# Kernel optimization log

Measured on AMD Instinct MI355X. Metric: run time of the kernel, lower is better.

## Reference

```python
import jax, jax.numpy as jnp
import numpy as np

EMBED_DIM = 1024
NUM_HEADS = 16
HEAD_DIM = EMBED_DIM // NUM_HEADS


def setup_inputs() -> dict:
    key = jax.random.key(0)
    ks = jax.random.split(key, 7)
    B, N, C = 2, 2048, EMBED_DIM
    s = 1.0 / np.sqrt(C)
    return {
        "x": jax.random.normal(ks[0], (B, N, C), dtype=jnp.float32),
        "phase_signal": jax.random.uniform(ks[1], (B,), dtype=jnp.float32),
        "qkv_w": jax.random.normal(ks[2], (3 * C, C), dtype=jnp.float32) * s,
        "qkv_b": jnp.zeros((3 * C,), dtype=jnp.float32),
        "proj_w": jax.random.normal(ks[3], (C, C), dtype=jnp.float32) * s,
        "proj_b": jnp.zeros((C,), dtype=jnp.float32),
        "phase_weight": jnp.ones((NUM_HEADS,), dtype=jnp.float32),
    }


def reference(x, phase_signal, qkv_w, qkv_b, proj_w, proj_b, phase_weight):
    B, N, C = x.shape
    H, D = NUM_HEADS, HEAD_DIM
    # qkv projection: [B,N,3C] -> [3,B,H,N,D]
    qkv = (x @ qkv_w.T + qkv_b).reshape(B, N, 3, H, D)
    qkv = jnp.transpose(qkv, (2, 0, 3, 1, 4))
    q, k, v = qkv[0], qkv[1], qkv[2]
    attn = jnp.einsum("bhnd,bhmd->bhnm", q, k) * (D ** -0.5)
    # per-(batch, head) phase modulation applied before softmax
    phase_mod = phase_weight[None, :, None, None] * phase_signal[:, None, None, None]
    attn = attn * (1.0 + 0.2 * phase_mod)
    attn = jax.nn.softmax(attn, axis=-1)  # dropout is identity in eval mode
    out = jnp.einsum("bhnm,bhmd->bhnd", attn, v)
    out = jnp.transpose(out, (0, 2, 1, 3)).reshape(B, N, C)
    return out @ proj_w.T + proj_b
```

## Files before the change

### kernel.cpp

```cpp
#include <hip/hip_runtime.h>
#include <stdint.h>

#define NUM_H 16
#define HD    64
#define CDIM  1024
#define NSEQ  2048
#define NBATCH 2
#define LOG2E 1.4426950408889634f

typedef __attribute__((ext_vector_type(8))) short short8;
typedef __attribute__((ext_vector_type(4))) float f32x4;
typedef __attribute__((ext_vector_type(16))) float f32x16;
typedef __attribute__((ext_vector_type(4))) unsigned short ushort4v;
typedef __attribute__((ext_vector_type(4))) float float4v;
typedef __attribute__((ext_vector_type(2))) unsigned int u32x2;

__device__ __forceinline__ unsigned short f2bf(float f) {
    unsigned int u = __builtin_bit_cast(unsigned int, f);
    unsigned int r = u + 0x7fffu + ((u >> 16) & 1u);
    return (unsigned short)(r >> 16);
}

__device__ __forceinline__ float bf2f(unsigned short u) {
    return __builtin_bit_cast(float, (unsigned int)u << 16);
}

__device__ __forceinline__ unsigned int cvtpk(float a, float b) {
    unsigned int r;
    asm("v_cvt_pk_bf16_f32 %0, %1, %2" : "=v"(r) : "v"(a), "v"(b));
    return r;
}

__device__ __forceinline__ void plswap(unsigned int &a, unsigned int &b) {
    asm("v_permlane32_swap_b32 %0, %1" : "+v"(a), "+v"(b));
}

__device__ __forceinline__ void gload_lds16(const void* g, const void* l) {
    __builtin_amdgcn_global_load_lds(
        (const __attribute__((address_space(1))) unsigned int*)(unsigned long long)(uintptr_t)g,
        (__attribute__((address_space(3))) unsigned int*)(unsigned int)(uintptr_t)l,
        16, 0, 0);
}

__global__ void cvt_all_kernel(const float* __restrict__ x,
                               const float* __restrict__ w1,
                               const float* __restrict__ wp,
                               unsigned short* __restrict__ xo,
                               unsigned short* __restrict__ w1o,
                               unsigned short* __restrict__ wpo) {
    int i = blockIdx.x * blockDim.x + threadIdx.x;
    const float* in; unsigned short* out;
    if (i < 1048576)      { in = x;  out = xo; }
    else if (i < 1835008) { in = w1; out = w1o; i -= 1048576; }
    else                  { in = wp; out = wpo; i -= 1835008; }
    float4v v = *(const float4v*)(in + (size_t)i * 4);
    ushort4v o;
    o[0] = f2bf(v[0]); o[1] = f2bf(v[1]); o[2] = f2bf(v[2]); o[3] = f2bf(v[3]);
    *(ushort4v*)(out + (size_t)i * 4) = o;
}

__global__ __launch_bounds__(512, 2) void gemm_qkv(
    const unsigned short* __restrict__ A,
    const unsigned short* __restrict__ Bw,
    const float* __restrict__ bias,
    const float* __restrict__ ps,
    const float* __restrict__ pw,
    unsigned short* __restrict__ qb,
    unsigned short* __restrict__ kfrag,
    unsigned short* __restrict__ vfrag)
{
    __shared__ unsigned short lds[2][2][2][128][64];

    const int tid = threadIdx.x;
    const int wid = tid >> 6;
    const int lane = tid & 63;
    const int l15 = lane & 15, l4 = lane >> 4;
    const int wave_m = wid >> 2, wave_n = wid & 3;

    const int bm = blockIdx.x;
    const int bn = blockIdx.y;

    f32x4 acc[8][4];
    const f32x4 zero4 = {0.f, 0.f, 0.f, 0.f};
#pragma unroll
    for (int m = 0; m < 8; ++m)
#pragma unroll
        for (int n = 0; n < 4; ++n) acc[m][n] = zero4;

    const int jr = lane >> 3;
    const int jc = ((lane & 7) ^ jr) << 4;
    const char* aB = (const char*)A  + (size_t)(bm * 256) * 2048;
    const char* bB = (const char*)Bw + (size_t)(bn * 256) * 2048;

    auto stageH = [&](int t, int which) {
        const int buf = t & 1;
        const int op = which >> 1, hf = which & 1;
        const char* src = (op == 0) ? aB : bB;
        const int rowb = hf * 128 + wid * 16;
        const size_t k0b = (size_t)t * 128;
        char* dst = (char*)&lds[buf][op][hf][wid * 16][0];
#pragma unroll
        for (int i = 0; i < 2; ++i)
            gload_lds16(src + (size_t)(rowb + i * 8 + jr) * 2048 + k0b + jc,
                        dst + i * 1024);
    };

    const int swz = (l15 & 7) << 4;
    auto rdA = [&](int buf, int mq, int mp, int kk) -> short8 {
        return *(const short8*)((const char*)&lds[buf][0][wave_m][mq * 64 + mp * 16 + l15][0]
                                + ((kk * 64 + l4 * 16) ^ swz));
    };
    auto rdB = [&](int buf, int nq, int np, int kk) -> short8 {
        const int br = wave_n * 64 + nq * 32 + np * 16 + l15;
        return *(const short8*)((const char*)&lds[buf][1][br >> 7][br & 127][0]
                                + ((kk * 64 + l4 * 16) ^ swz));
    };

    stageH(0, 0); stageH(0, 1); stageH(0, 2); stageH(0, 3);
    stageH(1, 2); stageH(1, 3); stageH(1, 0); stageH(1, 1);
    asm volatile("s_waitcnt vmcnt(8)" ::: "memory");
    __builtin_amdgcn_s_barrier();

    for (int t = 0; t < 16; ++t) {
        const int buf = t & 1;
        short8 af[4][2], bf[2][2][2];

#pragma unroll
        for (int mp = 0; mp < 4; ++mp) {
            af[mp][0] = rdA(buf, 0, mp, 0); af[mp][1] = rdA(buf, 0, mp, 1);
        }
#pragma unroll
        for (int np = 0; np < 2; ++np) {
            bf[0][np][0] = rdB(buf, 0, np, 0); bf[0][np][1] = rdB(buf, 0, np, 1);
        }
        __builtin_amdgcn_s_barrier();
        __builtin_amdgcn_s_setprio(1);
#pragma unroll
        for (int mp = 0; mp < 4; ++mp)
#pragma unroll
            for (int np = 0; np < 2; ++np)
#pragma unroll
                for (int kk = 0; kk < 2; ++kk)
                    acc[mp][np] = __builtin_amdgcn_mfma_f32_16x16x32_bf16(
                        af[mp][kk], bf[0][np][kk], acc[mp][np], 0, 0, 0);
        __builtin_amdgcn_s_setprio(0);
        __builtin_amdgcn_s_barrier();

#pragma unroll
        for (int np = 0; np < 2; ++np) {
            bf[1][np][0] = rdB(buf, 1, np, 0); bf[1][np][1] = rdB(buf, 1, np, 1);
        }
        if (t < 14) stageH(t + 2, 2);
        __builtin_amdgcn_s_barrier();
        __builtin_amdgcn_s_setprio(1);
#pragma unroll
        for (int mp = 0; mp < 4; ++mp)
#pragma unroll
            for (int np = 0; np < 2; ++np)
#pragma unroll
                for (int kk = 0; kk < 2; ++kk)
                    acc[mp][2 + np] = __builtin_amdgcn_mfma_f32_16x16x32_bf16(
                        af[mp][kk], bf[1][np][kk], acc[mp][2 + np], 0, 0, 0);
        __builtin_amdgcn_s_setprio(0);
        __builtin_amdgcn_s_barrier();

#pragma unroll
        for (int mp = 0; mp < 4; ++mp) {
            af[mp][0] = rdA(buf, 1, mp, 0); af[mp][1] = rdA(buf, 1, mp, 1);
        }
        if (t < 14) stageH(t + 2, 3);
        __builtin_amdgcn_s_barrier();
        __builtin_amdgcn_s_setprio(1);
#pragma unroll
        for (int mp = 0; mp < 4; ++mp)
#pragma unroll
            for (int np = 0; np < 2; ++np)
#pragma unroll
                for (int kk = 0; kk < 2; ++kk)
                    acc[4 + mp][np] = __builtin_amdgcn_mfma_f32_16x16x32_bf16(
                        af[mp][kk], bf[0][np][kk], acc[4 + mp][np], 0, 0, 0);
        __builtin_amdgcn_s_setprio(0);
        __builtin_amdgcn_s_barrier();

        if (t < 14) { stageH(t + 2, 0); stageH(t + 2, 1); }
        __builtin_amdgcn_s_barrier();
        __builtin_amdgcn_s_setprio(1);
#pragma unroll
        for (int mp = 0; mp < 4; ++mp)
#pragma unroll
            for (int np = 0; np < 2; ++np)
#pragma unroll
                for (int kk = 0; kk < 2; ++kk)
                    acc[4 + mp][2 + np] = __builtin_amdgcn_mfma_f32_16x16x32_bf16(
                        af[mp][kk], bf[1][np][kk], acc[4 + mp][2 + np], 0, 0, 0);
        __builtin_amdgcn_s_setprio(0);
        if (t < 14)       { asm volatile("s_waitcnt vmcnt(8)" ::: "memory"); }
        else if (t == 14) { asm volatile("s_waitcnt vmcnt(0)" ::: "memory"); }
        __builtin_amdgcn_s_barrier();
    }

    const int col_base = bn * 256 + wave_n * 64;
    const int t3b = bn >> 2;
    const int bb = bm >> 3;
    const int nn0 = (bm & 7) * 256;
    char* tbc = (char*)&lds[0][0][0][0][0];

    __syncthreads();

    if (t3b == 0) {
#pragma unroll
        for (int n = 0; n < 4; ++n) {
            const int d = n * 16 + l15;
            const float bv = bias[col_base + n * 16 + l15];
#pragma unroll
            for (int m = 0; m < 8; ++m) {
#pragma unroll
                for (int r = 0; r < 4; ++r) {
                    const int tt = wave_m * 128 + m * 16 + l4 * 4 + r;
                    *(unsigned short*)(tbc + wave_n * 32768 + tt * 128 +
                                       ((d * 2) ^ ((tt & 7) << 4))) = f2bf(acc[m][n][r] + bv);
                }
            }
        }
        __syncthreads();
#pragma unroll
        for (int i = 0; i < 16; ++i) {
            const int hq = i >> 2, sub = i & 3;
            const int tt = sub * 64 + (tid >> 3);
            const int chunk = tid & 7;
            const short8 v = *(const short8*)(tbc + hq * 32768 + tt * 128 +
                                              ((chunk * 16) ^ ((tt & 7) << 4)));
            *(short8*)(qb + ((size_t)(bb * 16 + bn * 4 + hq) * 2048 + nn0 + tt) * 64 + chunk * 8) = v;
        }
    } else if (t3b == 1) {
        const float ps0 = ps[0], ps1 = ps[1];
        const int hh = (bn - 4) * 4 + wave_n;
        const float kf = 0.125f * LOG2E *
                         (1.f + 0.2f * pw[hh] * ((bb == 0) ? ps0 : ps1));
#pragma unroll
        for (int n = 0; n < 4; ++n) {
            const int hi_ = l15 >> 3, e = l15 & 7;
            const float bv = bias[col_base + n * 16 + l15];
#pragma unroll
            for (int m = 0; m < 8; ++m) {
#pragma unroll
                for (int r = 0; r < 4; ++r) {
                    const int tt = wave_m * 128 + m * 16 + l4 * 4 + r;
                    const int ti = tt >> 6, u = tt & 63;
                    const int s_ = u >> 5, l31_ = u & 31;
                    *(unsigned short*)(tbc + (((wave_n * 4 + ti) * 8 + s_ * 4 + n) << 10) +
                                       ((hi_ * 32 + l31_) << 4) + e * 2) =
                        f2bf((acc[m][n][r] + bv) * kf);
                }
            }
        }
        __syncthreads();
#pragma unroll
        for (int i = 0; i < 16; ++i) {
            const int hq = i >> 2, ti = i & 3;
            const short8 v = *(const short8*)(tbc + i * 8192 + tid * 16);
            *(short8*)(kfrag + ((size_t)(bb * 16 + (bn - 4) * 4 + hq) * 32 +
                                ((bm & 7) * 4 + ti)) * 4096 + tid * 8) = v;
        }
    } else {
#pragma unroll
        for (int n = 0; n < 4; ++n) {
            const int d = n * 16 + l15;
            const int dt_ = n >> 1, l31_ = d & 31;
            const float bv = bias[col_base + n * 16 + l15];
#pragma unroll
            for (int m = 0; m < 8; ++m) {
#pragma unroll
                for (int r = 0; r < 4; ++r) {
                    const int tt = wave_m * 128 + m * 16 + l4 * 4 + r;
                    const int ti = tt >> 6, u = tt & 63;
                    const int ks = u >> 4, hi_ = (u >> 3) & 1, e = u & 7;
                    *(unsigned short*)(tbc + (((wave_n * 4 + ti) * 8 + dt_ * 4 + ks) << 10) +
                                       ((hi_ * 32 + l31_) << 4) + e * 2) =
                        f2bf(acc[m][n][r] + bv);
                }
            }
        }
        __syncthreads();
#pragma unroll
        for (int i = 0; i < 16; ++i) {
            const int hq = i >> 2, ti = i & 3;
            const short8 v = *(const short8*)(tbc + i * 8192 + tid * 16);
            *(short8*)(vfrag + ((size_t)(bb * 16 + (bn - 8) * 4 + hq) * 32 +
                                ((bm & 7) * 4 + ti)) * 4096 + tid * 8) = v;
        }
    }
}

__global__ __launch_bounds__(256, 2) void gemm_proj(
    const unsigned short* __restrict__ A,
    const unsigned short* __restrict__ Bw,
    const float* __restrict__ bias,
    float* __restrict__ out)
{
    __shared__ unsigned short As[2][128 * 64];
    __shared__ unsigned short Bs[2][128 * 64];
    const int tid = threadIdx.x;
    const int wid = tid >> 6;
    const int lane = tid & 63;
    const int l15 = lane & 15, l4 = lane >> 4;
    const int bm = blockIdx.x, bn = blockIdx.y;
    const int wr = wid >> 1, wc = wid & 1;

    f32x4 acc[4][4];
    const f32x4 zero4 = {0.f, 0.f, 0.f, 0.f};
#pragma unroll
    for (int m = 0; m < 4; ++m)
#pragma unroll
        for (int n = 0; n < 4; ++n) acc[m][n] = zero4;

    const int jr = lane >> 3;
    const int jc = ((lane & 7) ^ jr) << 4;
    const char* aB = (const char*)A  + (size_t)(bm * 128) * 2048;
    const char* bB = (const char*)Bw + (size_t)(bn * 128) * 2048;

    auto stage = [&](int buf, int k0) {
#pragma unroll
        for (int i = 0; i < 4; ++i) {
            const int rowb = wid * 32 + i * 8;
            gload_lds16(aB + (size_t)(rowb + jr) * 2048 + k0 * 2 + jc,
                        (const char*)&As[buf][0] + rowb * 128);
            gload_lds16(bB + (size_t)(rowb + jr) * 2048 + k0 * 2 + jc,
                        (const char*)&Bs[buf][0] + rowb * 128);
        }
    };

    const int swz = (l15 & 7) << 4;

    stage(0, 0);
    for (int it = 0; it < 16; ++it) {
        const int buf = it & 1;
        __syncthreads();
        if (it < 15) stage(buf ^ 1, (it + 1) * 64);
#pragma unroll
        for (int kk = 0; kk < 2; ++kk) {
            short8 a[4], b[4];
#pragma unroll
            for (int m = 0; m < 4; ++m)
                a[m] = *(const short8*)((const char*)&As[buf][0] +
                        (wr * 64 + m * 16 + l15) * 128 + ((kk * 64 + l4 * 16) ^ swz));
#pragma unroll
            for (int n = 0; n < 4; ++n)
                b[n] = *(const short8*)((const char*)&Bs[buf][0] +
                        (wc * 64 + n * 16 + l15) * 128 + ((kk * 64 + l4 * 16) ^ swz));
            __builtin_amdgcn_s_setprio(1);
#pragma unroll
            for (int m = 0; m < 4; ++m)
#pragma unroll
                for (int n = 0; n < 4; ++n)
                    acc[m][n] = __builtin_amdgcn_mfma_f32_16x16x32_bf16(a[m], b[n], acc[m][n], 0, 0, 0);
            __builtin_amdgcn_s_setprio(0);
        }
    }

    const int row_base = bm * 128 + wr * 64;
    const int col_base = bn * 128 + wc * 64;
#pragma unroll
    for (int n = 0; n < 4; ++n) {
        const int col = col_base + n * 16 + l15;
        const float bv = bias[col];
#pragma unroll
        for (int m = 0; m < 4; ++m) {
#pragma unroll
            for (int r = 0; r < 4; ++r) {
                const int row = row_base + m * 16 + l4 * 4 + r;
                out[(size_t)row * 1024 + col] = acc[m][n][r] + bv;
            }
        }
    }
}

__global__ __launch_bounds__(256, 4) void attn_kernel(
    const unsigned short* __restrict__ qb,
    const unsigned short* __restrict__ kfrag,
    const unsigned short* __restrict__ vfrag,
    unsigned short* __restrict__ o0,
    unsigned short* __restrict__ o1,
    float* __restrict__ lrb)
{
    __shared__ unsigned short KVs[2][2][4096];

    const int tid = threadIdx.x;
    const int w = tid >> 6;
    const int l = tid & 63;
    const int l31 = l & 31;
    const int hi = l >> 5;

    const int bid = blockIdx.y * 32 + blockIdx.x;
    const int wg = (bid & 7) * 128 + (bid >> 3);
    const int bh = wg >> 5;
    const int r5 = wg & 31;
    const int qt = r5 >> 1, kvh = r5 & 1;
    const int b = bh >> 4, h = bh & 15;
    const int q0 = qt * 128 + w * 32;

    const char* qg = (const char*)(qb + (size_t)bh * 2048 * 64);
    const unsigned short* kg = kfrag + ((size_t)bh * 32 + kvh * 16) * 4096;
    const unsigned short* vg = vfrag + ((size_t)bh * 32 + kvh * 16) * 4096;

    short8 qf[4];
#pragma unroll
    for (int t = 0; t < 4; ++t)
        qf[t] = *(const short8*)(qg + (size_t)(q0 + l31) * 128 + t * 32 + hi * 16);

    f32x16 oacc[2];
#pragma unroll
    for (int dt = 0; dt < 2; ++dt)
#pragma unroll
        for (int r = 0; r < 16; ++r) oacc[dt][r] = 0.f;
    float lr = 0.f;

    auto stage = [&](int buf, int T) {
#pragma unroll
        for (int i = 0; i < 2; ++i) {
            const int c = w * 2 + i;
            gload_lds16(kg + (size_t)T * 4096 + c * 512 + l * 8, &KVs[buf][0][c * 512]);
            gload_lds16(vg + (size_t)T * 4096 + c * 512 + l * 8, &KVs[buf][1][c * 512]);
        }
    };

    stage(0, 0);
    __syncthreads();

    for (int it = 0; it < 16; ++it) {
        const int buf = it & 1;
        if (it < 15) stage(buf ^ 1, it + 1);

        const unsigned short* Kb = &KVs[buf][0][0];
        const unsigned short* Vb = &KVs[buf][1][0];

        f32x16 sa[2];
        __builtin_amdgcn_s_setprio(1);
#pragma unroll
        for (int s = 0; s < 2; ++s) {
#pragma unroll
            for (int r = 0; r < 16; ++r) sa[s][r] = 0.f;
#pragma unroll
            for (int t = 0; t < 4; ++t) {
                const short8 kf = *(const short8*)(Kb + (s * 4 + t) * 512 + l * 8);
                sa[s] = __builtin_amdgcn_mfma_f32_32x32x16_bf16(kf, qf[t], sa[s], 0, 0, 0);
            }
        }
        __builtin_amdgcn_s_setprio(0);

#pragma unroll
        for (int s = 0; s < 2; ++s)
#pragma unroll
            for (int r = 0; r < 16; ++r)
                sa[s][r] = __builtin_amdgcn_exp2f(sa[s][r] - 20.0f);

        float ts[16];
#pragma unroll
        for (int r = 0; r < 16; ++r) ts[r] = sa[0][r] + sa[1][r];
#pragma unroll
        for (int d = 8; d >= 1; d >>= 1)
#pragma unroll
            for (int r = 0; r < 8; ++r)
                if (r < d) ts[r] += ts[r + d];
        lr += ts[0] + __shfl_xor(ts[0], 32);

#pragma unroll
        for (int s = 0; s < 2; ++s) {
            unsigned int wv[8];
#pragma unroll
            for (int g = 0; g < 8; ++g)
                wv[g] = cvtpk(sa[s][g * 2], sa[s][g * 2 + 1]);
            plswap(wv[0], wv[2]); plswap(wv[1], wv[3]);
            plswap(wv[4], wv[6]); plswap(wv[5], wv[7]);
            union { unsigned int u[4]; short8 s8; } f0, f1;
            f0.u[0] = wv[0]; f0.u[1] = wv[1]; f0.u[2] = wv[2]; f0.u[3] = wv[3];
            f1.u[0] = wv[4]; f1.u[1] = wv[5]; f1.u[2] = wv[6]; f1.u[3] = wv[7];
            __builtin_amdgcn_s_setprio(1);
#pragma unroll
            for (int dt = 0; dt < 2; ++dt) {
                const short8 v0 = *(const short8*)(Vb + (dt * 4 + s * 2 + 0) * 512 + l * 8);
                oacc[dt] = __builtin_amdgcn_mfma_f32_32x32x16_bf16(v0, f0.s8, oacc[dt], 0, 0, 0);
                const short8 v1 = *(const short8*)(Vb + (dt * 4 + s * 2 + 1) * 512 + l * 8);
                oacc[dt] = __builtin_amdgcn_mfma_f32_32x32x16_bf16(v1, f1.s8, oacc[dt], 0, 0, 0);
            }
            __builtin_amdgcn_s_setprio(0);
        }
        __syncthreads();
    }

    const float inv = 1.0f / lr;
    unsigned short* ob = kvh ? o1 : o0;
    char* outp = (char*)ob + ((size_t)(b * 2048 + q0 + l31) * 1024 + h * 64) * 2;
#pragma unroll
    for (int dt = 0; dt < 2; ++dt)
#pragma unroll
        for (int rg = 0; rg < 4; ++rg) {
            u32x2 pkd;
            pkd[0] = cvtpk(oacc[dt][rg * 4 + 0] * inv, oacc[dt][rg * 4 + 1] * inv);
            pkd[1] = cvtpk(oacc[dt][rg * 4 + 2] * inv, oacc[dt][rg * 4 + 3] * inv);
            *(u32x2*)(outp + (size_t)(dt * 32 + rg * 8 + hi * 4) * 2) = pkd;
        }
    if (hi == 0)
        lrb[(kvh << 16) + (bh << 11) + q0 + l31] = lr;
}

__global__ void combine_kernel(unsigned short* __restrict__ o0,
                               const unsigned short* __restrict__ o1,
                               const float* __restrict__ lrb) {
    const int idx = blockIdx.x * blockDim.x + threadIdx.x;
    const size_t e0 = (size_t)idx * 8;
    const int row = (int)(e0 >> 10);
    const int col = (int)(e0 & 1023);
    const int b = row >> 11, q = row & 2047, h = col >> 6;
    const int bhq = ((b * 16 + h) << 11) + q;
    const float l0 = lrb[bhq], l1 = lrb[65536 + bhq];
    const float w0 = l0 / (l0 + l1);
    const float w1 = 1.0f - w0;
    short8 v0 = *(short8*)(o0 + e0);
    const short8 v1 = *(const short8*)(o1 + e0);
    short8 o;
#pragma unroll
    for (int j = 0; j < 8; ++j)
        o[j] = (short)f2bf(bf2f((unsigned short)v0[j]) * w0 +
                           bf2f((unsigned short)v1[j]) * w1);
    *(short8*)(o0 + e0) = o;
}

extern "C" void kernel_launch(void* const* d_in, const int* in_sizes, int n_in,
                              void* d_out, int out_size, void* d_ws, size_t ws_size,
                              hipStream_t stream) {
    const float* x      = (const float*)d_in[0];
    const float* ps     = (const float*)d_in[1];
    const float* qkv_w  = (const float*)d_in[2];
    const float* qkv_b  = (const float*)d_in[3];
    const float* proj_w = (const float*)d_in[4];
    const float* proj_b = (const float*)d_in[5];
    const float* pw     = (const float*)d_in[6];
    float* out = (float*)d_out;
    char* ws = (char*)d_ws;

    unsigned short* x_bf    = (unsigned short*)(ws);
    unsigned short* w1_bf   = (unsigned short*)(ws + (8u  << 20));
    unsigned short* wp_bf   = (unsigned short*)(ws + (14u << 20));
    unsigned short* qb      = (unsigned short*)(ws + (16u << 20));
    unsigned short* kfrag   = (unsigned short*)(ws + (24u << 20));
    unsigned short* vfrag   = (unsigned short*)(ws + (32u << 20));
    unsigned short* o1      = (unsigned short*)(ws + (40u << 20));
    unsigned short* o0      = x_bf;
    float*          lrb     = (float*)w1_bf;
    unsigned short* attn_bf = o0;

    cvt_all_kernel<<<8192, 256, 0, stream>>>(x, qkv_w, proj_w, x_bf, w1_bf, wp_bf);
    gemm_qkv<<<dim3(16, 12), 512, 0, stream>>>(x_bf, w1_bf, qkv_b, ps, pw, qb, kfrag, vfrag);
    attn_kernel<<<dim3(32, 32), 256, 0, stream>>>(qb, kfrag, vfrag, o0, o1, lrb);
    combine_kernel<<<2048, 256, 0, stream>>>(o0, o1, lrb);
    gemm_proj<<<dim3(32, 8), 256, 0, stream>>>(attn_bf, wp_bf, proj_b, out);
}
```

Before: 113.0 us.

## Fuse split-KV combine into projection GEMM A-staging and merge QKV GEMM phases

Removes the separate combine kernel by having the projection GEMM load both partial attention outputs and their softmax row sums, blend them in registers and write the bf16 result into LDS as its A tile. This drops one kernel launch and a full read-modify-write round trip of the attention output. In exchange, A staging now uses ordinary loads and ALU work instead of async global-to-LDS copies, and that work is repeated across the 8 column blocks. The QKV GEMM main loop is also regrouped from four barrier-separated MFMA phases into two, loading all B fragments up front and issuing stage copies around a single barrier.

```diff
diff --git a/kernel.cpp b/kernel.cpp
--- a/kernel.cpp
+++ b/kernel.cpp
@@ -130,9 +130,11 @@
             af[mp][0] = rdA(buf, 0, mp, 0); af[mp][1] = rdA(buf, 0, mp, 1);
         }
 #pragma unroll
-        for (int np = 0; np < 2; ++np) {
-            bf[0][np][0] = rdB(buf, 0, np, 0); bf[0][np][1] = rdB(buf, 0, np, 1);
-        }
+        for (int nq = 0; nq < 2; ++nq)
+#pragma unroll
+            for (int np = 0; np < 2; ++np) {
+                bf[nq][np][0] = rdB(buf, nq, np, 0); bf[nq][np][1] = rdB(buf, nq, np, 1);
+            }
         __builtin_amdgcn_s_barrier();
         __builtin_amdgcn_s_setprio(1);
 #pragma unroll
@@ -143,16 +145,6 @@
                 for (int kk = 0; kk < 2; ++kk)
                     acc[mp][np] = __builtin_amdgcn_mfma_f32_16x16x32_bf16(
                         af[mp][kk], bf[0][np][kk], acc[mp][np], 0, 0, 0);
-        __builtin_amdgcn_s_setprio(0);
-        __builtin_amdgcn_s_barrier();
-
-#pragma unroll
-        for (int np = 0; np < 2; ++np) {
-            bf[1][np][0] = rdB(buf, 1, np, 0); bf[1][np][1] = rdB(buf, 1, np, 1);
-        }
-        if (t < 14) stageH(t + 2, 2);
-        __builtin_amdgcn_s_barrier();
-        __builtin_amdgcn_s_setprio(1);
 #pragma unroll
         for (int mp = 0; mp < 4; ++mp)
 #pragma unroll
@@ -168,8 +160,10 @@
         for (int mp = 0; mp < 4; ++mp) {
             af[mp][0] = rdA(buf, 1, mp, 0); af[mp][1] = rdA(buf, 1, mp, 1);
         }
-        if (t < 14) stageH(t + 2, 3);
+        if (t < 14) { stageH(t + 2, 2); stageH(t + 2, 3); }
+        asm volatile("s_waitcnt lgkmcnt(0)" ::: "memory");
         __builtin_amdgcn_s_barrier();
+        if (t < 14) { stageH(t + 2, 0); stageH(t + 2, 1); }
         __builtin_amdgcn_s_setprio(1);
 #pragma unroll
         for (int mp = 0; mp < 4; ++mp)
@@ -179,12 +173,6 @@
                 for (int kk = 0; kk < 2; ++kk)
                     acc[4 + mp][np] = __builtin_amdgcn_mfma_f32_16x16x32_bf16(
                         af[mp][kk], bf[0][np][kk], acc[4 + mp][np], 0, 0, 0);
-        __builtin_amdgcn_s_setprio(0);
-        __builtin_amdgcn_s_barrier();
-
-        if (t < 14) { stageH(t + 2, 0); stageH(t + 2, 1); }
-        __builtin_amdgcn_s_barrier();
-        __builtin_amdgcn_s_setprio(1);
 #pragma unroll
         for (int mp = 0; mp < 4; ++mp)
 #pragma unroll
@@ -293,7 +281,9 @@
 }
 
 __global__ __launch_bounds__(256, 2) void gemm_proj(
-    const unsigned short* __restrict__ A,
+    const unsigned short* __restrict__ o0,
+    const unsigned short* __restrict__ o1,
+    const float* __restrict__ lrb,
     const unsigned short* __restrict__ Bw,
     const float* __restrict__ bias,
     float* __restrict__ out)
@@ -316,27 +306,48 @@
 
     const int jr = lane >> 3;
     const int jc = ((lane & 7) ^ jr) << 4;
-    const char* aB = (const char*)A  + (size_t)(bm * 128) * 2048;
     const char* bB = (const char*)Bw + (size_t)(bn * 128) * 2048;
 
-    auto stage = [&](int buf, int k0) {
+    auto stageB = [&](int buf, int k0) {
 #pragma unroll
         for (int i = 0; i < 4; ++i) {
             const int rowb = wid * 32 + i * 8;
-            gload_lds16(aB + (size_t)(rowb + jr) * 2048 + k0 * 2 + jc,
-                        (const char*)&As[buf][0] + rowb * 128);
             gload_lds16(bB + (size_t)(rowb + jr) * 2048 + k0 * 2 + jc,
                         (const char*)&Bs[buf][0] + rowb * 128);
         }
     };
 
+    auto stageA = [&](int buf, int k0) {
+        const int h = k0 >> 6;
+#pragma unroll
+        for (int i = 0; i < 4; ++i) {
+            const int row_local = wid * 32 + i * 8 + jr;
+            const int grow = bm * 128 + row_local;
+            const int b_ = grow >> 11, q_ = grow & 2047;
+            const int idx = ((b_ * 16 + h) << 11) + q_;
+            const float l0 = lrb[idx];
+            const float l1 = lrb[65536 + idx];
+            const float w0 = l0 / (l0 + l1);
+            const float w1 = 1.0f - w0;
+            const size_t goff = (size_t)grow * 1024 + k0 + (jc >> 1);
+            const short8 v0 = *(const short8*)(o0 + goff);
+            const short8 v1 = *(const short8*)(o1 + goff);
+            short8 bl;
+#pragma unroll
+            for (int j = 0; j < 8; ++j)
+                bl[j] = (short)f2bf(bf2f((unsigned short)v0[j]) * w0 +
+                                    bf2f((unsigned short)v1[j]) * w1);
+            *(short8*)((char*)&As[buf][0] + row_local * 128 + (lane & 7) * 16) = bl;
+        }
+    };
+
     const int swz = (l15 & 7) << 4;
 
-    stage(0, 0);
+    stageB(0, 0); stageA(0, 0);
     for (int it = 0; it < 16; ++it) {
         const int buf = it & 1;
         __syncthreads();
-        if (it < 15) stage(buf ^ 1, (it + 1) * 64);
+        if (it < 15) { stageB(buf ^ 1, (it + 1) * 64); stageA(buf ^ 1, (it + 1) * 64); }
 #pragma unroll
         for (int kk = 0; kk < 2; ++kk) {
             short8 a[4], b[4];
@@ -502,28 +513,6 @@
         }
     if (hi == 0)
         lrb[(kvh << 16) + (bh << 11) + q0 + l31] = lr;
-}
-
-__global__ void combine_kernel(unsigned short* __restrict__ o0,
-                               const unsigned short* __restrict__ o1,
-                               const float* __restrict__ lrb) {
-    const int idx = blockIdx.x * blockDim.x + threadIdx.x;
-    const size_t e0 = (size_t)idx * 8;
-    const int row = (int)(e0 >> 10);
-    const int col = (int)(e0 & 1023);
-    const int b = row >> 11, q = row & 2047, h = col >> 6;
-    const int bhq = ((b * 16 + h) << 11) + q;
-    const float l0 = lrb[bhq], l1 = lrb[65536 + bhq];
-    const float w0 = l0 / (l0 + l1);
-    const float w1 = 1.0f - w0;
-    short8 v0 = *(short8*)(o0 + e0);
-    const short8 v1 = *(const short8*)(o1 + e0);
-    short8 o;
-#pragma unroll
-    for (int j = 0; j < 8; ++j)
-        o[j] = (short)f2bf(bf2f((unsigned short)v0[j]) * w0 +
-                           bf2f((unsigned short)v1[j]) * w1);
-    *(short8*)(o0 + e0) = o;
 }
 
 extern "C" void kernel_launch(void* const* d_in, const int* in_sizes, int n_in,
@@ -548,11 +537,9 @@
     unsigned short* o1      = (unsigned short*)(ws + (40u << 20));
     unsigned short* o0      = x_bf;
     float*          lrb     = (float*)w1_bf;
-    unsigned short* attn_bf = o0;
 
     cvt_all_kernel<<<8192, 256, 0, stream>>>(x, qkv_w, proj_w, x_bf, w1_bf, wp_bf);
     gemm_qkv<<<dim3(16, 12), 512, 0, stream>>>(x_bf, w1_bf, qkv_b, ps, pw, qb, kfrag, vfrag);
     attn_kernel<<<dim3(32, 32), 256, 0, stream>>>(qb, kfrag, vfrag, o0, o1, lrb);
-    combine_kernel<<<2048, 256, 0, stream>>>(o0, o1, lrb);
-    gemm_proj<<<dim3(32, 8), 256, 0, stream>>>(attn_bf, wp_bf, proj_b, out);
-}
+    gemm_proj<<<dim3(32, 8), 256, 0, stream>>>(o0, o1, lrb, wp_bf, proj_b, out);
+}
```

Result: slower. 127.5 us (+12.8%).
